# Performance work log

Hardware: AMD Instinct MI355X
Metric: run time of the kernel (lower is better)

The kernel has to match this reference:

```python
import jax, jax.numpy as jnp
import numpy as np

B, T, D = 4, 2048, 1024
H, HD = 16, 64  # num_heads, head_size; H*HD == D
DFF = 4 * D
EPS = 1e-5

def _ln(x, g, b):
    mu = jnp.mean(x, axis=-1, keepdims=True)
    var = jnp.mean(jnp.square(x - mu), axis=-1, keepdims=True)
    return (x - mu) * jax.lax.rsqrt(var + EPS) * g + b

def setup_inputs() -> dict:
    key = jax.random.key(0)
    ks = jax.random.split(key, 12)
    s = lambda fan_in: 1.0 / np.sqrt(fan_in)
    return {
        "x": jax.random.normal(ks[0], (B, T, D), jnp.float32),
        "Wq": jax.random.normal(ks[1], (H, D, HD), jnp.float32) * s(D),
        "Wk": jax.random.normal(ks[2], (H, D, HD), jnp.float32) * s(D),
        "Wv": jax.random.normal(ks[3], (H, D, HD), jnp.float32) * s(D),
        "Wo": jax.random.normal(ks[4], (D, D), jnp.float32) * s(D),
        "bo": jax.random.normal(ks[5], (D,), jnp.float32) * 0.01,
        "W1": jax.random.normal(ks[6], (D, DFF), jnp.float32) * s(D),
        "b1": jax.random.normal(ks[7], (DFF,), jnp.float32) * 0.01,
        "W2": jax.random.normal(ks[8], (DFF, D), jnp.float32) * s(DFF),
        "b2": jax.random.normal(ks[9], (D,), jnp.float32) * 0.01,
        "g1": jnp.ones((D,), jnp.float32),
        "be1": jnp.zeros((D,), jnp.float32),
        "g2": jnp.ones((D,), jnp.float32),
        "be2": jnp.zeros((D,), jnp.float32),
    }

def reference(x, Wq, Wk, Wv, Wo, bo, W1, b1, W2, b2, g1, be1, g2, be2):
    # pre-LN attention
    h = _ln(x, g1, be1)                                   # [B,T,D]
    q = jnp.einsum('btd,hde->bhte', h, Wq)                # [B,H,T,HD]
    k = jnp.einsum('btd,hde->bhte', h, Wk)
    v = jnp.einsum('btd,hde->bhte', h, Wv)
    scores = jnp.einsum('bhte,bhse->bhts', q, k) * (HD ** -0.5)  # [B,H,T,T]
    mask = jnp.tril(jnp.ones((T, T), bool))
    scores = jnp.where(mask, scores, -jnp.inf)
    attn = jax.nn.softmax(scores, axis=-1)
    ctx = jnp.einsum('bhts,bhse->bhte', attn, v)          # [B,H,T,HD]
    ctx = ctx.transpose(0, 2, 1, 3).reshape(B, T, D)      # concat heads
    x = x + jnp.einsum('btd,de->bte', ctx, Wo) + bo
    # pre-LN FFN
    h2 = _ln(x, g2, be2)
    ff = jax.nn.relu(jnp.einsum('btd,df->btf', h2, W1) + b1)
    x = x + jnp.einsum('btf,fd->btd', ff, W2) + b2
    return x
```

## Files before the change

### kernel.cpp

```cpp
#include <hip/hip_runtime.h>
#include <stdint.h>

#define B_ 4
#define T_ 2048
#define D_ 1024
#define H_ 16
#define HD_ 64
#define DFF_ 4096
#define M_ (B_ * T_)

typedef __bf16 bf16x8 __attribute__((ext_vector_type(8)));
typedef float f32x4 __attribute__((ext_vector_type(4)));

__device__ __forceinline__ uint16_t f2bf(float f) {
  union { float f; uint32_t u; } v;
  v.f = f;
  uint32_t r = v.u + 0x7FFF + ((v.u >> 16) & 1);
  return (uint16_t)(r >> 16);
}

#define GLD_LDS(gp, lp)                                                        \
  __builtin_amdgcn_global_load_lds(                                            \
      (const __attribute__((address_space(1))) void*)(gp),                     \
      (__attribute__((address_space(3))) void*)(lp), 16, 0, 0)

__global__ __launch_bounds__(256) void ln_bf16(const float* __restrict__ x,
                                               const float* __restrict__ gamma,
                                               const float* __restrict__ beta,
                                               uint16_t* __restrict__ out) {
  __shared__ float red[4];
  const int tid = threadIdx.x;
  const size_t row = blockIdx.x;
  const float4 v = ((const float4*)(x + row * D_))[tid];
  float s = v.x + v.y + v.z + v.w;
#pragma unroll
  for (int off = 32; off >= 1; off >>= 1) s += __shfl_xor(s, off, 64);
  if ((tid & 63) == 0) red[tid >> 6] = s;
  __syncthreads();
  const float mean = (red[0] + red[1] + red[2] + red[3]) * (1.0f / D_);
  const float d0 = v.x - mean, d1 = v.y - mean, d2 = v.z - mean, d3 = v.w - mean;
  float ss = d0 * d0 + d1 * d1 + d2 * d2 + d3 * d3;
#pragma unroll
  for (int off = 32; off >= 1; off >>= 1) ss += __shfl_xor(ss, off, 64);
  __syncthreads();
  if ((tid & 63) == 0) red[tid >> 6] = ss;
  __syncthreads();
  const float var = (red[0] + red[1] + red[2] + red[3]) * (1.0f / D_);
  const float rstd = rsqrtf(var + 1e-5f);
  const float4 g = ((const float4*)gamma)[tid];
  const float4 b = ((const float4*)beta)[tid];
  ushort4 o;
  o.x = f2bf(d0 * rstd * g.x + b.x);
  o.y = f2bf(d1 * rstd * g.y + b.y);
  o.z = f2bf(d2 * rstd * g.z + b.z);
  o.w = f2bf(d3 * rstd * g.w + b.w);
  ((ushort4*)(out + row * D_))[tid] = o;
}

__global__ __launch_bounds__(256) void transpose_cast(const float* __restrict__ in,
                                                      uint16_t* __restrict__ out,
                                                      int R, int C) {
  __shared__ float tile[32][33];
  const int tx = threadIdx.x & 31, ty = threadIdx.x >> 5;
  const int c0 = blockIdx.x * 32, r0 = blockIdx.y * 32;
#pragma unroll
  for (int i = 0; i < 32; i += 8)
    tile[ty + i][tx] = in[(size_t)(r0 + ty + i) * C + c0 + tx];
  __syncthreads();
#pragma unroll
  for (int i = 0; i < 32; i += 8)
    out[(size_t)(c0 + ty + i) * R + r0 + tx] = f2bf(tile[tx][ty + i]);
}

__global__ __launch_bounds__(256) void qkv_wt(const float* __restrict__ Wq,
                                              const float* __restrict__ Wk,
                                              const float* __restrict__ Wv,
                                              uint16_t* __restrict__ out) {
  __shared__ float tile[32][33];
  const int tx = threadIdx.x & 31, ty = threadIdx.x >> 5;
  const int z = blockIdx.z, which = z >> 4, hh = z & 15;
  const float* W = (which == 0) ? Wq : ((which == 1) ? Wk : Wv);
  const float* in = W + (size_t)hh * D_ * HD_;
  const int e0 = blockIdx.x * 32, d0 = blockIdx.y * 32;
#pragma unroll
  for (int i = 0; i < 32; i += 8)
    tile[ty + i][tx] = in[(size_t)(d0 + ty + i) * HD_ + e0 + tx];
  __syncthreads();
#pragma unroll
  for (int i = 0; i < 32; i += 8)
    out[((size_t)(which * 1024 + hh * 64) + e0 + ty + i) * D_ + d0 + tx] =
        f2bf(tile[tx][ty + i]);
}

template <int BN>
__global__ __launch_bounds__(256) void gemm_bf16(const uint16_t* __restrict__ A,
                                                 const uint16_t* __restrict__ Bt,
                                                 void* __restrict__ C,
                                                 const float* __restrict__ bias,
                                                 const float* __restrict__ resid,
                                                 int M, int N, int K, int lda,
                                                 int ldb, int flags) {
  constexpr int NJ = BN / 32;
  __shared__ __align__(16) uint16_t As[128 * 64];
  __shared__ __align__(16) uint16_t Bs[BN * 64];
  const int tid = threadIdx.x;
  const int lane = tid & 63, w = tid >> 6;
  const int quad = lane >> 4, lr = lane & 15;
  const int wr = w >> 1, wc = w & 1;

  const int n_tiles = N / BN;
  const int pid = blockIdx.x;
  const int grp = 16 * n_tiles;
  const int gid = pid / grp;
  const int rem = pid - gid * grp;
  const int nt = rem / 16;
  const int mt = gid * 16 + (rem - nt * 16);
  const int bn0 = nt * BN, bm0 = mt * 128;

  f32x4 acc[4][NJ];
#pragma unroll
  for (int i = 0; i < 4; i++)
#pragma unroll
    for (int j = 0; j < NJ; j++) acc[i][j] = f32x4{0.f, 0.f, 0.f, 0.f};

  const int s_row = lane >> 3, s_slot = lane & 7;

  for (int k0 = 0; k0 < K; k0 += 64) {
#pragma unroll
    for (int u = 0; u < 4; u++) {
      const int r = w * 32 + u * 8 + s_row;
      const int cg = s_slot ^ (r & 7);
      GLD_LDS(A + (size_t)(bm0 + r) * lda + k0 + cg * 8, As + (w * 32 + u * 8) * 64);
    }
#pragma unroll
    for (int u = 0; u < NJ; u++) {
      const int r = w * (BN / 4) + u * 8 + s_row;
      const int cg = s_slot ^ (r & 7);
      GLD_LDS(Bt + (size_t)(bn0 + r) * ldb + k0 + cg * 8,
              Bs + (w * (BN / 4) + u * 8) * 64);
    }
    __syncthreads();

#pragma unroll
    for (int ks = 0; ks < 2; ks++) {
      bf16x8 af[4], bfr[NJ];
#pragma unroll
      for (int i = 0; i < 4; i++) {
        const int m = wr * 64 + i * 16 + lr;
        const int slot = (ks * 4 + quad) ^ (m & 7);
        af[i] = *(const bf16x8*)(As + m * 64 + slot * 8);
      }
#pragma unroll
      for (int j = 0; j < NJ; j++) {
        const int n = wc * (BN / 2) + j * 16 + lr;
        const int slot = (ks * 4 + quad) ^ (n & 7);
        bfr[j] = *(const bf16x8*)(Bs + n * 64 + slot * 8);
      }
#pragma unroll
      for (int i = 0; i < 4; i++)
#pragma unroll
        for (int j = 0; j < NJ; j++)
          acc[i][j] =
              __builtin_amdgcn_mfma_f32_16x16x32_bf16(af[i], bfr[j], acc[i][j], 0, 0, 0);
    }
    __syncthreads();
  }

  const int base_m = bm0 + wr * 64 + quad * 4;
  const int base_n = bn0 + wc * (BN / 2) + lr;
#pragma unroll
  for (int i = 0; i < 4; i++) {
#pragma unroll
    for (int j = 0; j < NJ; j++) {
      const int col = base_n + j * 16;
      const float bv = bias ? bias[col] : 0.f;
#pragma unroll
      for (int r = 0; r < 4; r++) {
        const size_t row = base_m + i * 16 + r;
        float v = acc[i][j][r] + bv;
        if (resid) v += resid[row * N + col];
        if (flags & 1) v = fmaxf(v, 0.f);
        if (flags & 2)
          ((uint16_t*)C)[row * N + col] = f2bf(v);
        else
          ((float*)C)[row * N + col] = v;
      }
    }
  }
}

__global__ __launch_bounds__(256) void v_transpose(const uint16_t* __restrict__ qkv,
                                                   uint16_t* __restrict__ vtb) {
  __shared__ __align__(16) uint16_t tile[64 * 72];
  const int tid = threadIdx.x;
  const int t0 = blockIdx.x * 64;
  const int bh = blockIdx.y;
  const int b = bh >> 4, h = bh & 15;
  const uint16_t* src = qkv + (size_t)b * T_ * 3072 + 2048 + h * 64;
#pragma unroll
  for (int u = 0; u < 2; u++) {
    const int uu = tid + u * 256;
    const int r = uu >> 3, c = uu & 7;
    *(int4*)(tile + r * 72 + c * 8) =
        *(const int4*)(src + (size_t)(t0 + r) * 3072 + c * 8);
  }
  __syncthreads();
  uint16_t* dst = vtb + ((size_t)bh * 64) * T_ + t0;
#pragma unroll
  for (int u = 0; u < 2; u++) {
    const int uu = tid + u * 256;
    const int e = uu >> 3, c2 = uu & 7;
    union { uint16_t u16[8]; int4 v; } tmp;
#pragma unroll
    for (int jj = 0; jj < 8; jj++) tmp.u16[jj] = tile[(c2 * 8 + jj) * 72 + e];
    *(int4*)(dst + (size_t)e * T_ + c2 * 8) = tmp.v;
  }
}

__global__ __launch_bounds__(256) void attn_mfma(const uint16_t* __restrict__ qkv,
                                                 const uint16_t* __restrict__ vtb,
                                                 uint16_t* __restrict__ ctx) {
  __shared__ __align__(16) uint16_t Ks[64 * 64];
  __shared__ __align__(16) uint16_t Vt[64 * 64];
  __shared__ __align__(16) uint16_t Ps[128 * 72];
  const int tid = threadIdx.x;
  const int lane = tid & 63, w = tid >> 6;
  const int quad = lane >> 4, lr = lane & 15;
  const int lr7 = lr & 7;
  const int h = blockIdx.y, b = blockIdx.z;
  const uint16_t* base = qkv + (size_t)b * T_ * 3072 + h * 64;
  const uint16_t* vbase = vtb + ((size_t)(b * H_ + h) * 64) * T_;
  const int s_row = lane >> 3, s_slot = lane & 7;

#pragma unroll
  for (int half = 0; half < 2; half++) {
    const int tq = (half == 0) ? (int)blockIdx.x : 15 - (int)blockIdx.x;
    const int q0 = tq * 128;

    bf16x8 aq[2][2];
#pragma unroll
    for (int i = 0; i < 2; i++)
#pragma unroll
      for (int ks = 0; ks < 2; ks++)
        aq[i][ks] = *(const bf16x8*)(base + (size_t)(q0 + w * 32 + i * 16 + lr) * 3072 +
                                     ks * 32 + quad * 8);

    f32x4 oacc[2][4];
#pragma unroll
    for (int i = 0; i < 2; i++)
#pragma unroll
      for (int j = 0; j < 4; j++) oacc[i][j] = f32x4{0.f, 0.f, 0.f, 0.f};
    float l_part[2] = {0.f, 0.f};

    const int row_min_w = q0 + w * 32;
    const int row_max_w = row_min_w + 31;
    const int nstg = 2 * tq + 2;

    for (int st = 0; st < nstg; st++) {
      __syncthreads();
#pragma unroll
      for (int u = 0; u < 2; u++) {
        const int r = w * 16 + u * 8 + s_row;
        const int cg = s_slot ^ (r & 7);
        GLD_LDS(base + 1024 + (size_t)(st * 64 + r) * 3072 + cg * 8,
                Ks + (w * 16 + u * 8) * 64);
        GLD_LDS(vbase + (size_t)r * T_ + st * 64 + cg * 8, Vt + (w * 16 + u * 8) * 64);
      }
      __syncthreads();

      if (st * 64 > row_max_w) continue;

      f32x4 sa[2][4];
#pragma unroll
      for (int i = 0; i < 2; i++)
#pragma unroll
        for (int sf = 0; sf < 4; sf++) sa[i][sf] = f32x4{0.f, 0.f, 0.f, 0.f};
#pragma unroll
      for (int ks = 0; ks < 2; ks++) {
        bf16x8 ak[4];
#pragma unroll
        for (int sf = 0; sf < 4; sf++) {
          const int slot = (ks * 4 + quad) ^ lr7;
          ak[sf] = *(const bf16x8*)(Ks + (sf * 16 + lr) * 64 + slot * 8);
        }
#pragma unroll
        for (int i = 0; i < 2; i++)
#pragma unroll
          for (int sf = 0; sf < 4; sf++)
            sa[i][sf] = __builtin_amdgcn_mfma_f32_16x16x32_bf16(ak[sf], aq[i][ks],
                                                                sa[i][sf], 0, 0, 0);
      }

      const bool diag = (st * 64 + 63 > row_min_w);
      if (diag) {
#pragma unroll
        for (int i = 0; i < 2; i++) {
          const int mrow = q0 + w * 32 + i * 16 + lr;
#pragma unroll
          for (int sf = 0; sf < 4; sf++) {
            const int s0 = st * 64 + sf * 16 + quad * 4;
            float p[4];
#pragma unroll
            for (int r = 0; r < 4; r++) {
              float sv = sa[i][sf][r];
              if (s0 + r > mrow) sv = -1e30f;
              p[r] = exp2f(fmaf(sv, 0.18033688f, -28.8539008f));
              l_part[i] += p[r];
            }
            ushort4 pk;
            pk.x = f2bf(p[0]);
            pk.y = f2bf(p[1]);
            pk.z = f2bf(p[2]);
            pk.w = f2bf(p[3]);
            *(ushort4*)(Ps + (size_t)(w * 32 + i * 16 + lr) * 72 + sf * 16 + quad * 4) =
                pk;
          }
        }
      } else {
#pragma unroll
        for (int i = 0; i < 2; i++) {
#pragma unroll
          for (int sf = 0; sf < 4; sf++) {
            float p[4];
#pragma unroll
            for (int r = 0; r < 4; r++) {
              p[r] = exp2f(fmaf(sa[i][sf][r], 0.18033688f, -28.8539008f));
              l_part[i] += p[r];
            }
            ushort4 pk;
            pk.x = f2bf(p[0]);
            pk.y = f2bf(p[1]);
            pk.z = f2bf(p[2]);
            pk.w = f2bf(p[3]);
            *(ushort4*)(Ps + (size_t)(w * 32 + i * 16 + lr) * 72 + sf * 16 + quad * 4) =
                pk;
          }
        }
      }

#pragma unroll
      for (int ks = 0; ks < 2; ks++) {
        bf16x8 ap[2], bv[4];
#pragma unroll
        for (int i = 0; i < 2; i++)
          ap[i] = *(const bf16x8*)(Ps + (size_t)(w * 32 + i * 16 + lr) * 72 + ks * 32 +
                                   quad * 8);
#pragma unroll
        for (int j = 0; j < 4; j++) {
          const int slot = (ks * 4 + quad) ^ lr7;
          bv[j] = *(const bf16x8*)(Vt + (j * 16 + lr) * 64 + slot * 8);
        }
#pragma unroll
        for (int i = 0; i < 2; i++)
#pragma unroll
          for (int j = 0; j < 4; j++)
            oacc[i][j] =
                __builtin_amdgcn_mfma_f32_16x16x32_bf16(ap[i], bv[j], oacc[i][j], 0, 0, 0);
      }
    }

    float linv[2];
#pragma unroll
    for (int i = 0; i < 2; i++) {
      float l = l_part[i];
      l += __shfl_xor(l, 16, 64);
      l += __shfl_xor(l, 32, 64);
      linv[i] = 1.f / l;
    }
    uint16_t* ob =
        ctx + ((size_t)b * T_ + q0 + w * 32 + quad * 4) * D_ + h * 64 + lr;
#pragma unroll
    for (int i = 0; i < 2; i++)
#pragma unroll
      for (int r = 0; r < 4; r++) {
        const float inv = __shfl(linv[i], quad * 4 + r, 64);
#pragma unroll
        for (int j = 0; j < 4; j++)
          ob[(size_t)(i * 16 + r) * D_ + j * 16] = f2bf(oacc[i][j][r] * inv);
      }
  }
}

extern "C" void kernel_launch(void* const* d_in, const int* in_sizes, int n_in,
                              void* d_out, int out_size, void* d_ws, size_t ws_size,
                              hipStream_t stream) {
  const float* x = (const float*)d_in[0];
  const float* Wq = (const float*)d_in[1];
  const float* Wk = (const float*)d_in[2];
  const float* Wv = (const float*)d_in[3];
  const float* Wo = (const float*)d_in[4];
  const float* bo = (const float*)d_in[5];
  const float* W1 = (const float*)d_in[6];
  const float* b1 = (const float*)d_in[7];
  const float* W2 = (const float*)d_in[8];
  const float* b2 = (const float*)d_in[9];
  const float* g1 = (const float*)d_in[10];
  const float* be1 = (const float*)d_in[11];
  const float* g2 = (const float*)d_in[12];
  const float* be2 = (const float*)d_in[13];
  float* out = (float*)d_out;

  const size_t MB = 1024ull * 1024ull;
  if (ws_size < 200 * MB) return;
  char* ws = (char*)d_ws;
  uint16_t* hbuf = (uint16_t*)(ws + 0 * MB);
  uint16_t* wqkvt = (uint16_t*)(ws + 16 * MB);
  uint16_t* wot = (uint16_t*)(ws + 22 * MB);
  uint16_t* w1t = (uint16_t*)(ws + 24 * MB);
  uint16_t* w2t = (uint16_t*)(ws + 32 * MB);
  float* x1 = (float*)(ws + 40 * MB);
  uint16_t* qkvb = (uint16_t*)(ws + 72 * MB);
  uint16_t* ctxb = (uint16_t*)(ws + 120 * MB);
  uint16_t* vtb = (uint16_t*)(ws + 136 * MB);
  uint16_t* ffb = (uint16_t*)(ws + 136 * MB);

  qkv_wt<<<dim3(2, 32, 48), 256, 0, stream>>>(Wq, Wk, Wv, wqkvt);
  transpose_cast<<<dim3(32, 32), 256, 0, stream>>>(Wo, wot, 1024, 1024);
  transpose_cast<<<dim3(128, 32), 256, 0, stream>>>(W1, w1t, 1024, 4096);
  transpose_cast<<<dim3(32, 128), 256, 0, stream>>>(W2, w2t, 4096, 1024);

  ln_bf16<<<M_, 256, 0, stream>>>(x, g1, be1, hbuf);
  gemm_bf16<128><<<64 * 24, 256, 0, stream>>>(hbuf, wqkvt, qkvb, nullptr, nullptr,
                                              M_, 3 * D_, D_, D_, D_, 2);
  v_transpose<<<dim3(T_ / 64, B_ * H_), 256, 0, stream>>>(qkvb, vtb);
  attn_mfma<<<dim3(8, H_, B_), 256, 0, stream>>>(qkvb, vtb, ctxb);
  gemm_bf16<64><<<64 * 16, 256, 0, stream>>>(ctxb, wot, x1, bo, x, M_, D_, D_, D_,
                                             D_, 0);
  ln_bf16<<<M_, 256, 0, stream>>>(x1, g2, be2, hbuf);
  gemm_bf16<128><<<64 * 32, 256, 0, stream>>>(hbuf, w1t, ffb, b1, nullptr, M_, DFF_,
                                              D_, D_, D_, 1 | 2);
  gemm_bf16<64><<<64 * 16, 256, 0, stream>>>(ffb, w2t, out, b2, x1, M_, D_, DFF_,
                                             DFF_, DFF_, 0);
}
```

Before: 553.8 us.

## Double-buffer K/V tiles in attention and merge weight-prep kernels into one launch

The attention kernel now keeps two K/V LDS buffers and issues the global-to-LDS loads for the next key block before computing on the current one. This replaces the load-then-barrier-then-compute pattern and aims to hide load latency. Separately, the four weight transpose/cast launches are merged into one kernel that picks its task from the block index, saving launch overhead. The double buffer drops the barrier that waited for the loads to land, so correctness depends on the loads being complete when the next iteration reads them, which is a synchronisation risk. It also doubles the K/V LDS footprint.

```diff
diff --git a/kernel.cpp b/kernel.cpp
--- a/kernel.cpp
+++ b/kernel.cpp
@@ -57,12 +57,47 @@
   ((ushort4*)(out + row * D_))[tid] = o;
 }
 
-__global__ __launch_bounds__(256) void transpose_cast(const float* __restrict__ in,
-                                                      uint16_t* __restrict__ out,
-                                                      int R, int C) {
+__global__ __launch_bounds__(256) void prep_weights(
+    const float* __restrict__ Wq, const float* __restrict__ Wk,
+    const float* __restrict__ Wv, const float* __restrict__ Wo,
+    const float* __restrict__ W1, const float* __restrict__ W2,
+    uint16_t* __restrict__ wqkvt, uint16_t* __restrict__ wot,
+    uint16_t* __restrict__ w1t, uint16_t* __restrict__ w2t) {
   __shared__ float tile[32][33];
   const int tx = threadIdx.x & 31, ty = threadIdx.x >> 5;
-  const int c0 = blockIdx.x * 32, r0 = blockIdx.y * 32;
+  const int pid = blockIdx.x;
+
+  if (pid >= 9216) {
+    const int p = pid - 9216;
+    const int bx = p & 1, by = (p >> 1) & 31, z = p >> 6;
+    const int which = z >> 4, hh = z & 15;
+    const float* W = (which == 0) ? Wq : ((which == 1) ? Wk : Wv);
+    const float* in = W + (size_t)hh * D_ * HD_;
+    const int e0 = bx * 32, d0 = by * 32;
+#pragma unroll
+    for (int i = 0; i < 32; i += 8)
+      tile[ty + i][tx] = in[(size_t)(d0 + ty + i) * HD_ + e0 + tx];
+    __syncthreads();
+#pragma unroll
+    for (int i = 0; i < 32; i += 8)
+      wqkvt[((size_t)(which * 1024 + hh * 64) + e0 + ty + i) * D_ + d0 + tx] =
+          f2bf(tile[tx][ty + i]);
+    return;
+  }
+
+  const float* in;
+  uint16_t* out;
+  int R, C, bx, by;
+  if (pid < 1024) {
+    in = Wo; out = wot; R = 1024; C = 1024; bx = pid & 31; by = pid >> 5;
+  } else if (pid < 5120) {
+    const int p = pid - 1024;
+    in = W1; out = w1t; R = 1024; C = 4096; bx = p & 127; by = p >> 7;
+  } else {
+    const int p = pid - 5120;
+    in = W2; out = w2t; R = 4096; C = 1024; bx = p & 31; by = p >> 5;
+  }
+  const int c0 = bx * 32, r0 = by * 32;
 #pragma unroll
   for (int i = 0; i < 32; i += 8)
     tile[ty + i][tx] = in[(size_t)(r0 + ty + i) * C + c0 + tx];
@@ -70,26 +105,6 @@
 #pragma unroll
   for (int i = 0; i < 32; i += 8)
     out[(size_t)(c0 + ty + i) * R + r0 + tx] = f2bf(tile[tx][ty + i]);
-}
-
-__global__ __launch_bounds__(256) void qkv_wt(const float* __restrict__ Wq,
-                                              const float* __restrict__ Wk,
-                                              const float* __restrict__ Wv,
-                                              uint16_t* __restrict__ out) {
-  __shared__ float tile[32][33];
-  const int tx = threadIdx.x & 31, ty = threadIdx.x >> 5;
-  const int z = blockIdx.z, which = z >> 4, hh = z & 15;
-  const float* W = (which == 0) ? Wq : ((which == 1) ? Wk : Wv);
-  const float* in = W + (size_t)hh * D_ * HD_;
-  const int e0 = blockIdx.x * 32, d0 = blockIdx.y * 32;
-#pragma unroll
-  for (int i = 0; i < 32; i += 8)
-    tile[ty + i][tx] = in[(size_t)(d0 + ty + i) * HD_ + e0 + tx];
-  __syncthreads();
-#pragma unroll
-  for (int i = 0; i < 32; i += 8)
-    out[((size_t)(which * 1024 + hh * 64) + e0 + ty + i) * D_ + d0 + tx] =
-        f2bf(tile[tx][ty + i]);
 }
 
 template <int BN>
@@ -220,8 +235,8 @@
 __global__ __launch_bounds__(256) void attn_mfma(const uint16_t* __restrict__ qkv,
                                                  const uint16_t* __restrict__ vtb,
                                                  uint16_t* __restrict__ ctx) {
-  __shared__ __align__(16) uint16_t Ks[64 * 64];
-  __shared__ __align__(16) uint16_t Vt[64 * 64];
+  __shared__ __align__(16) uint16_t Ks[2][64 * 64];
+  __shared__ __align__(16) uint16_t Vt[2][64 * 64];
   __shared__ __align__(16) uint16_t Ps[128 * 72];
   const int tid = threadIdx.x;
   const int lane = tid & 63, w = tid >> 6;
@@ -256,19 +271,34 @@
     const int row_max_w = row_min_w + 31;
     const int nstg = 2 * tq + 2;
 
+    __syncthreads();
+#pragma unroll
+    for (int u = 0; u < 2; u++) {
+      const int r = w * 16 + u * 8 + s_row;
+      const int cg = s_slot ^ (r & 7);
+      GLD_LDS(base + 1024 + (size_t)r * 3072 + cg * 8, Ks[0] + (w * 16 + u * 8) * 64);
+      GLD_LDS(vbase + (size_t)r * T_ + cg * 8, Vt[0] + (w * 16 + u * 8) * 64);
+    }
+
     for (int st = 0; st < nstg; st++) {
       __syncthreads();
-#pragma unroll
-      for (int u = 0; u < 2; u++) {
-        const int r = w * 16 + u * 8 + s_row;
-        const int cg = s_slot ^ (r & 7);
-        GLD_LDS(base + 1024 + (size_t)(st * 64 + r) * 3072 + cg * 8,
-                Ks + (w * 16 + u * 8) * 64);
-        GLD_LDS(vbase + (size_t)r * T_ + st * 64 + cg * 8, Vt + (w * 16 + u * 8) * 64);
-      }
-      __syncthreads();
+      if (st + 1 < nstg) {
+        uint16_t* Kb = Ks[(st + 1) & 1];
+        uint16_t* Vb = Vt[(st + 1) & 1];
+#pragma unroll
+        for (int u = 0; u < 2; u++) {
+          const int r = w * 16 + u * 8 + s_row;
+          const int cg = s_slot ^ (r & 7);
+          GLD_LDS(base + 1024 + (size_t)((st + 1) * 64 + r) * 3072 + cg * 8,
+                  Kb + (w * 16 + u * 8) * 64);
+          GLD_LDS(vbase + (size_t)r * T_ + (st + 1) * 64 + cg * 8,
+                  Vb + (w * 16 + u * 8) * 64);
+        }
+      }
 
       if (st * 64 > row_max_w) continue;
+      const uint16_t* Kb = Ks[st & 1];
+      const uint16_t* Vb = Vt[st & 1];
 
       f32x4 sa[2][4];
 #pragma unroll
@@ -281,7 +311,7 @@
 #pragma unroll
         for (int sf = 0; sf < 4; sf++) {
           const int slot = (ks * 4 + quad) ^ lr7;
-          ak[sf] = *(const bf16x8*)(Ks + (sf * 16 + lr) * 64 + slot * 8);
+          ak[sf] = *(const bf16x8*)(Kb + (sf * 16 + lr) * 64 + slot * 8);
         }
 #pragma unroll
         for (int i = 0; i < 2; i++)
@@ -348,7 +378,7 @@
 #pragma unroll
         for (int j = 0; j < 4; j++) {
           const int slot = (ks * 4 + quad) ^ lr7;
-          bv[j] = *(const bf16x8*)(Vt + (j * 16 + lr) * 64 + slot * 8);
+          bv[j] = *(const bf16x8*)(Vb + (j * 16 + lr) * 64 + slot * 8);
         }
 #pragma unroll
         for (int i = 0; i < 2; i++)
@@ -414,11 +444,8 @@
   uint16_t* vtb = (uint16_t*)(ws + 136 * MB);
   uint16_t* ffb = (uint16_t*)(ws + 136 * MB);
 
-  qkv_wt<<<dim3(2, 32, 48), 256, 0, stream>>>(Wq, Wk, Wv, wqkvt);
-  transpose_cast<<<dim3(32, 32), 256, 0, stream>>>(Wo, wot, 1024, 1024);
-  transpose_cast<<<dim3(128, 32), 256, 0, stream>>>(W1, w1t, 1024, 4096);
-  transpose_cast<<<dim3(32, 128), 256, 0, stream>>>(W2, w2t, 4096, 1024);
-
+  prep_weights<<<12288, 256, 0, stream>>>(Wq, Wk, Wv, Wo, W1, W2, wqkvt, wot, w1t,
+                                          w2t);
   ln_bf16<<<M_, 256, 0, stream>>>(x, g1, be1, hbuf);
   gemm_bf16<128><<<64 * 24, 256, 0, stream>>>(hbuf, wqkvt, qkvb, nullptr, nullptr,
                                               M_, 3 * D_, D_, D_, D_, 2);
```

Result: no change. 552.7 us (-0.2%).
